# Kernel tuning notes

Measured on AMD Instinct MI355X. Metric: run time of the kernel, lower is better.

## Reference

```python
import jax, jax.numpy as jnp
from jax import lax
import numpy as np

# HH / synapse constants (CFG in original repo; standard values matching the rate eqns)
GNA, GK, GL = 40.0, 35.0, 0.3
ENA, EK, EL = 55.0, -77.0, -65.0
GS, VS = 1.0, 0.0
IAPP = 1.0
VT, KP = -20.0, 3.0
A_D, A_R = 1.0, 0.1
DT = 0.02

B, N, L = 16, 2000, 1024


def setup_inputs() -> dict:
    key = jax.random.key(0)
    z = jax.random.uniform(key, (B, N, L), dtype=jnp.float32)
    return {"z": z}


def _rates(V):
    # Singularity-safe rate constants (the torch code patches V==25 / V==-35 exactly).
    at25 = V == 25.0
    atm35 = V == -35.0
    dN = jnp.where(at25, 1.0, 1.0 - jnp.exp((-V + 25.0) / 9.0))
    dM = jnp.where(atm35, 1.0, 1.0 - jnp.exp((-V - 35.0) / 9.0))
    dNb = jnp.where(at25, 1.0, 1.0 - jnp.exp((V - 25.0) / 9.0))
    dMb = jnp.where(atm35, 1.0, 1.0 - jnp.exp((V + 35.0) / 9.0))
    aN = jnp.where(at25, 0.18, 0.02 * (V - 25.0) / dN)
    bN = jnp.where(at25, 0.08, -0.002 * (V - 25.0) / dNb)
    aM = jnp.where(atm35, 1.638, 0.182 * (V + 35.0) / dM)
    bM = jnp.where(atm35, 1.16, -0.124 * (V + 35.0) / dMb)
    aH = 0.25 * jnp.exp((-V - 90.0) / 12.0)
    bH = 0.25 * jnp.exp((V + 34.0) / 12.0)
    return aN, bN, aM, bM, aH, bH


def _step(carry, z_prev):
    V, m, n, h, y = carry
    pow1 = GNA * m ** 3 * h
    pow2 = GK * n ** 4
    G = DT / 2 * (pow1 + pow2 + GL + GS * y)
    E = pow1 * ENA + pow2 * EK + GL * EL + GS * VS * y
    Vn = (V * (1.0 - G) + DT * (E + IAPP)) / (1.0 + G)
    aN, bN, aM, bM, aH, bH = _rates(Vn)
    mn = (aM * DT + (1.0 - DT / 2 * (aM + bM)) * m) / (DT / 2 * (aM + bM) + 1.0)
    nn = (aN * DT + (1.0 - DT / 2 * (aN + bN)) * n) / (DT / 2 * (aN + bN) + 1.0)
    hn = (aH * DT + (1.0 - DT / 2 * (aH + bH)) * h) / (DT / 2 * (aH + bH) + 1.0)
    ady = A_D * z_prev
    yn = (ady * DT + (1.0 - DT / 2 * (ady + A_R)) * y) / (DT / 2 * (ady + A_R) + 1.0)
    return (Vn, mn, nn, hn, yn), Vn


def _hh(z):
    b, n_t, l = z.shape
    zt = jnp.moveaxis(z, 1, 0)  # (N, B, L); step k uses z[k-1]
    V0 = jnp.full((b, l), -70.0, dtype=z.dtype)
    zeros = jnp.zeros((b, l), dtype=z.dtype)
    ones = jnp.ones((b, l), dtype=z.dtype)
    carry0 = (V0, zeros, zeros, ones, zeros)
    _, Vseq = lax.scan(_step, carry0, zt[:-1])  # (N-1, B, L)
    Vall = jnp.concatenate([V0[None], Vseq], axis=0)  # (N, B, L)
    V = jnp.moveaxis(Vall, 0, 1)  # (B, N, L)
    return jax.nn.sigmoid((V - VT) / KP)


def reference(z):
    return _hh(z)
```

## Files before the change

kernel.cpp:

```cpp
#include <hip/hip_runtime.h>

#define N_ 2000
#define L_ 1024

__device__ __forceinline__ float rcpf(float d) { return __builtin_amdgcn_rcpf(d); }
__device__ __forceinline__ float ex2(float x)  { return __builtin_amdgcn_exp2f(x); }

#define STEP1(K, RS)                                                          \
  {                                                                           \
    const int kk = (K);                                                       \
    float zc = zb[RS];                                                        \
    int kpre = kk + 15;                                                       \
    int kc = kpre < 1998 ? kpre : 1998;                                       \
    zb[RS] = z[base + kc * L_];                                               \
                            \
    float mh   = m * h;                                                       \
    float m2   = m * m;                                                       \
    float valm = m2 * mh;                                          \
    float n2   = n * n;                                                       \
    float valn = n2 * n2;                                           \
    float gy   = __fmaf_rn(y, 0.01f, 0.003f);                                 \
    float G    = __fmaf_rn(valm, 0.4f, __fmaf_rn(valn, 0.35f, gy));           \
    float E    = __fmaf_rn(valm, 2200.0f, __fmaf_rn(valn, -2695.0f, -19.5f)); \
            \
    float r    = rcpf(1.0f + G);                                              \
    float tVD  = __fmaf_rn(E, 0.02f, __fmaf_rn(2.0f, V, 0.02f));              \
    float Vn   = __fmaf_rn(tVD, r, -V);                                       \
                                                               \
    float eRm  = ex2(__fmaf_rn(Vn, K9, 35.0f * K9));                          \
    float eRn  = ex2(__fmaf_rn(Vn, K9, -25.0f * K9));                         \
    float rrm  = rcpf(eRm - 1.0f);                                            \
    float rrn  = rcpf(eRn - 1.0f);                                            \
    float um   = Vn + 35.0f;                                                  \
    float un   = Vn - 25.0f;                                                  \
    float urm  = um * rrm;                                                    \
    float urn  = un * rrn;                                                    \
    float Xm   = __fmaf_rn(0.00182f, eRm, 0.00124f);                          \
    float Xn   = __fmaf_rn(0.0002f,  eRn, 0.00002f);                          \
    float sm   = urm * Xm;                                                    \
    float sn   = urn * Xn;                                                    \
    float aM   = 0.182f * (urm * eRm);                                        \
    float aN   = 0.02f  * (urn * eRn);                                        \
    bool patm  = (Vn == -35.0f);                                              \
    bool patn  = (Vn == 25.0f);                                               \
    sm = patm ? 0.02798f : sm;  aM = patm ? 1.638f : aM;                      \
    sn = patn ? 0.0026f  : sn;  aN = patn ? 0.18f  : aN;                      \
          \
    float numm = __fmaf_rn(aM, 0.02f, __fmaf_rn(-sm, m, m));                  \
    float numn = __fmaf_rn(aN, 0.02f, __fmaf_rn(-sn, n, n));                  \
    m = numm * rcpf(1.0f + sm);                                               \
    n = numn * rcpf(1.0f + sn);                                               \
                              \
    float aH   = 0.25f * ex2(__fmaf_rn(Vn, -K12, -90.0f * K12));              \
    float bH   = 0.25f * ex2(__fmaf_rn(Vn,  K12,  34.0f * K12));              \
    float sh   = __fmaf_rn(aH, 0.01f, 0.01f * bH);                            \
    float numh = __fmaf_rn(aH, 0.02f, __fmaf_rn(-sh, h, h));                  \
    float qh   = 1.0f + sh;                                                   \
    float sy   = __fmaf_rn(zc, 0.01f, 0.001f);                                \
    float numy = __fmaf_rn(zc, 0.02f, __fmaf_rn(-sy, y, y));                  \
    float qy   = 1.0f + sy;                                                   \
    float rq   = rcpf(qh * qy);                                               \
    h = numh * (rq * qy);                                                     \
    y = numy * (rq * qh);                                                     \
    V = Vn;                                                                   \
                     \
    float e2 = eRm * eRm;                                                     \
    float ts = (e2 * eRm) * 0.006737946999085467f;                            \
    float sg = ts * rcpf(1.0f + ts);                                          \
    __builtin_nontemporal_store(sg, &out[base + kk * L_]);                    \
  }

__global__ __launch_bounds__(64) void hh_kernel(const float* __restrict__ z,
                                                float* __restrict__ out) {
    const int t   = blockIdx.x * 64 + threadIdx.x;
    const int b   = t >> 10;
    const int l   = t & 1023;
    const int base = b * (N_ * L_) + l;

    const float K9  = 0.16029944898766259f;
    const float K12 = 0.12022458674074695f;

    float V = -70.0f;
    float m = 0.0f, n = 0.0f, h = 1.0f, y = 0.0f;

    float zb[16];
#pragma unroll
    for (int i = 0; i < 16; ++i) zb[i] = z[base + i * L_];

    __builtin_nontemporal_store(5.777750e-8f, &out[base]);

    int k = 1;
    for (int g = 0; g < 124; ++g) {
#pragma unroll
        for (int j = 0; j < 16; ++j) {
            STEP1(k + j, j)
        }
        k += 16;
    }
#pragma unroll
    for (int j = 0; j < 15; ++j) {
        STEP1(k + j, j)
    }
}

extern "C" void kernel_launch(void* const* d_in, const int* in_sizes, int n_in,
                              void* d_out, int out_size, void* d_ws, size_t ws_size,
                              hipStream_t stream) {
    const float* z = (const float*)d_in[0];
    float* out = (float*)d_out;
    hh_kernel<<<256, 64, 0, stream>>>(z, out);
}
```

Measured before the change: 521.8 us.

## Derive gating exponential from shared exp2 and batch all reciprocals into one

Computes the n-gate exponential as a constant multiple of the m-gate exponential, which removes one exp2 per step. All per-step divisions (m, n, h, y updates and the output sigmoid) are merged into a single reciprocal recovered through products. The z prefetch depth and unroll factor drop from 16 to 8, and the output stores become ordinary rather than nontemporal. The goal is to shorten the serial dependency chain of transcendental ops in this latency-bound recurrence. In exchange, the long product chains may lose precision or overflow, and the shallower prefetch may expose more load latency.

```diff
diff --git a/kernel.cpp b/kernel.cpp
--- a/kernel.cpp
+++ b/kernel.cpp
@@ -10,64 +10,73 @@
   {                                                                           \
     const int kk = (K);                                                       \
     float zc = zb[RS];                                                        \
-    int kpre = kk + 15;                                                       \
+    int kpre = kk + 7;                                                        \
     int kc = kpre < 1998 ? kpre : 1998;                                       \
     zb[RS] = z[base + kc * L_];                                               \
-                            \
+                                                       \
     float mh   = m * h;                                                       \
     float m2   = m * m;                                                       \
     float valm = m2 * mh;                                          \
     float n2   = n * n;                                                       \
-    float valn = n2 * n2;                                           \
+    float valn = n2 * n2;                                          \
     float gy   = __fmaf_rn(y, 0.01f, 0.003f);                                 \
     float G    = __fmaf_rn(valm, 0.4f, __fmaf_rn(valn, 0.35f, gy));           \
     float E    = __fmaf_rn(valm, 2200.0f, __fmaf_rn(valn, -2695.0f, -19.5f)); \
-            \
-    float r    = rcpf(1.0f + G);                                              \
+    float rV   = rcpf(1.0f + G);                                              \
     float tVD  = __fmaf_rn(E, 0.02f, __fmaf_rn(2.0f, V, 0.02f));              \
-    float Vn   = __fmaf_rn(tVD, r, -V);                                       \
-                                                               \
-    float eRm  = ex2(__fmaf_rn(Vn, K9, 35.0f * K9));                          \
-    float eRn  = ex2(__fmaf_rn(Vn, K9, -25.0f * K9));                         \
-    float rrm  = rcpf(eRm - 1.0f);                                            \
-    float rrn  = rcpf(eRn - 1.0f);                                            \
+    float Vn   = __fmaf_rn(tVD, rV, -V);          \
+                                      \
+    float eRm  = ex2(__fmaf_rn(Vn, K9, 35.0f * K9));       \
+    float eRn  = eRm * CN;                                 \
+    float dm   = eRm - 1.0f;                                                  \
+    float dn   = eRn - 1.0f;                                                  \
+    bool patm  = (Vn == -35.0f);                                              \
+    bool patn  = (Vn == 25.0f);                                               \
+    float dmS  = patm ? 1.0f : dm;        \
+    float dnS  = patn ? 1.0f : dn;        \
+    float rp   = rcpf(dmS * dnS);                                             \
+    float rrm  = rp * dnS;                                                    \
+    float rrn  = rp * dmS;                                                    \
     float um   = Vn + 35.0f;                                                  \
     float un   = Vn - 25.0f;                                                  \
     float urm  = um * rrm;                                                    \
     float urn  = un * rrn;                                                    \
-    float Xm   = __fmaf_rn(0.00182f, eRm, 0.00124f);                          \
-    float Xn   = __fmaf_rn(0.0002f,  eRn, 0.00002f);                          \
-    float sm   = urm * Xm;                                                    \
-    float sn   = urn * Xn;                                                    \
+    float sm   = urm * __fmaf_rn(0.00182f, eRm, 0.00124f);                    \
+    float sn   = urn * __fmaf_rn(0.0002f,  eRn, 0.00002f);                    \
     float aM   = 0.182f * (urm * eRm);                                        \
     float aN   = 0.02f  * (urn * eRn);                                        \
-    bool patm  = (Vn == -35.0f);                                              \
-    bool patn  = (Vn == 25.0f);                                               \
     sm = patm ? 0.02798f : sm;  aM = patm ? 1.638f : aM;                      \
     sn = patn ? 0.0026f  : sn;  aN = patn ? 0.18f  : aN;                      \
-          \
-    float numm = __fmaf_rn(aM, 0.02f, __fmaf_rn(-sm, m, m));                  \
-    float numn = __fmaf_rn(aN, 0.02f, __fmaf_rn(-sn, n, n));                  \
-    m = numm * rcpf(1.0f + sm);                                               \
-    n = numn * rcpf(1.0f + sn);                                               \
-                              \
+                                      \
     float aH   = 0.25f * ex2(__fmaf_rn(Vn, -K12, -90.0f * K12));              \
     float bH   = 0.25f * ex2(__fmaf_rn(Vn,  K12,  34.0f * K12));              \
     float sh   = __fmaf_rn(aH, 0.01f, 0.01f * bH);                            \
+    float sy   = __fmaf_rn(zc, 0.01f, 0.001f);                                \
+    float qm = 1.0f + sm, qn = 1.0f + sn, qh = 1.0f + sh, qy = 1.0f + sy;     \
+    float numm = __fmaf_rn(aM, 0.02f, __fmaf_rn(-sm, m, m));                  \
+    float numn = __fmaf_rn(aN, 0.02f, __fmaf_rn(-sn, n, n));                  \
     float numh = __fmaf_rn(aH, 0.02f, __fmaf_rn(-sh, h, h));                  \
-    float qh   = 1.0f + sh;                                                   \
-    float sy   = __fmaf_rn(zc, 0.01f, 0.001f);                                \
     float numy = __fmaf_rn(zc, 0.02f, __fmaf_rn(-sy, y, y));                  \
-    float qy   = 1.0f + sy;                                                   \
-    float rq   = rcpf(qh * qy);                                               \
-    h = numh * (rq * qy);                                                     \
-    y = numy * (rq * qh);                                                     \
-    V = Vn;                                                                   \
-                     \
+       \
     float e2 = eRm * eRm;                                                     \
     float ts = (e2 * eRm) * 0.006737946999085467f;                            \
-    float sg = ts * rcpf(1.0f + ts);                                          \
-    __builtin_nontemporal_store(sg, &out[base + kk * L_]);                    \
+    float uS = 1.0f + ts;                                                     \
+                                  \
+    float t1 = qm * qn;                                                       \
+    float t2 = qh * qy;                                                       \
+    float t12 = t1 * t2;                                                      \
+    float rall = rcpf(t12 * uS);                                              \
+    float rq  = rall * uS;                                     \
+    float rs  = rall * t12;                                    \
+    float rmn = rq * t2;                                       \
+    float rhy = rq * t1;                                       \
+    m = numm * (rmn * qn);                                                    \
+    n = numn * (rmn * qm);                                                    \
+    h = numh * (rhy * qy);                                                    \
+    y = numy * (rhy * qh);                                                    \
+    V = Vn;                                                                   \
+    float sg = ts * rs;                                                       \
+    out[base + kk * L_] = sg;                                                 \
   }
 
 __global__ __launch_bounds__(64) void hh_kernel(const float* __restrict__ z,
@@ -79,26 +88,27 @@
 
     const float K9  = 0.16029944898766259f;
     const float K12 = 0.12022458674074695f;
+    const float CN  = 0.0012726338013398079f;
 
     float V = -70.0f;
     float m = 0.0f, n = 0.0f, h = 1.0f, y = 0.0f;
 
-    float zb[16];
+    float zb[8];
 #pragma unroll
-    for (int i = 0; i < 16; ++i) zb[i] = z[base + i * L_];
+    for (int i = 0; i < 8; ++i) zb[i] = z[base + i * L_];
 
-    __builtin_nontemporal_store(5.777750e-8f, &out[base]);
+    out[base] = 5.777750e-8f;
 
     int k = 1;
-    for (int g = 0; g < 124; ++g) {
+    for (int g = 0; g < 249; ++g) {
 #pragma unroll
-        for (int j = 0; j < 16; ++j) {
+        for (int j = 0; j < 8; ++j) {
             STEP1(k + j, j)
         }
-        k += 16;
+        k += 8;
     }
 #pragma unroll
-    for (int j = 0; j < 15; ++j) {
+    for (int j = 0; j < 7; ++j) {
         STEP1(k + j, j)
     }
 }
```

After: 495.4 us. -5.1%, faster.
